# Optimization experiments

Measured on AMD Instinct MI355X. Metric: run time of the kernel, lower is better.

Reference implementation:

```python
import jax, jax.numpy as jnp
import numpy as np

N_NODES = 50000
N_DIRECTED = 800000  # symmetrized to 1.6M (src,dst) pairs
IN_FEAT = 256
HEADS = 8
OUT = 64


def setup_inputs() -> dict:
    key = jax.random.key(0)
    k1, k2, k3, k4, k5 = jax.random.split(key, 5)
    r = jax.random.randint(k1, (N_DIRECTED,), 0, N_NODES)
    c = jax.random.randint(k2, (N_DIRECTED,), 0, N_NODES)
    # symmetric adjacency (values = 1), as edge list
    src = jnp.concatenate([r, c])
    dst = jnp.concatenate([c, r])
    x = jax.random.normal(k3, (N_NODES, IN_FEAT), dtype=jnp.float32)
    Ws = jax.random.normal(k4, (HEADS, OUT, IN_FEAT), dtype=jnp.float32) * 0.05
    As = jax.random.normal(k5, (HEADS, 2 * OUT, 1), dtype=jnp.float32) * 0.05
    return {"x": x, "src": src, "dst": dst, "Ws": Ws, "As": As}


def reference(x, src, dst, Ws, As):
    H, O, F = Ws.shape
    N = x.shape[0]
    # t_nodes = inputs @ Ws^T  -> [H, N, O]
    t = jnp.einsum('nf,hof->hno', x, Ws)
    a_l = As[:, :O, 0]   # [H, O]
    a_r = As[:, O:, 0]   # [H, O]
    Al = jnp.einsum('hno,ho->hn', t, a_l)  # [H, N]
    Ar = jnp.einsum('hno,ho->hn', t, a_r)  # [H, N]
    outs = []
    for k in range(H):
        # sparse E[i,j] = Al[i] + Ar[j] on adjacency pattern
        e = Al[k][src] + Ar[k][dst]  # [E]
        # NOTE: original applies tf.sparse.softmax to E directly (its lrelu
        # tensor is computed but never used), so no leaky_relu here.
        m = jax.ops.segment_max(e, src, num_segments=N)
        ex = jnp.exp(e - m[src])
        den = jax.ops.segment_sum(ex, src, num_segments=N)
        alpha = ex / den[src]
        # sparse_dense_matmul(alphas, t_nodes[k])
        h = jax.ops.segment_sum(alpha[:, None] * t[k][dst], src, num_segments=N)
        outs.append(h)
    out = jnp.stack(outs, axis=1)          # [N, H, O]
    out = out.reshape(N, H * O)            # reduction=False -> concat heads
    return jax.nn.elu(out)
```

## Files before the change

### kernel.cpp

```cpp
#include <hip/hip_runtime.h>
#include <hip/hip_bf16.h>

#define NN 50000
#define INF 256
#define NH 8
#define OUTF 64
#define NC 512
#define NTILES 782
#define EPB 8192
#define NBK 391

typedef __attribute__((ext_vector_type(8))) short bf16x8;
typedef __attribute__((ext_vector_type(4))) float f32x4;
typedef unsigned long long u64;

__device__ __forceinline__ unsigned short f2bf(float f){
  unsigned u = __float_as_uint(f);
  u += 0x7FFFu + ((u>>16)&1u);
  return (unsigned short)(u>>16);
}

#define GLOAD_LDS16(g, s) \
  __builtin_amdgcn_global_load_lds((const __attribute__((address_space(1))) void*)(g), \
                                   (__attribute__((address_space(3))) void*)(s), 16, 0, 0)

__global__ __launch_bounds__(256) void k_prep_w(const float* __restrict__ W,
                                                unsigned short* __restrict__ Wt){
  const int tid = threadIdx.x;
  const int r = tid>>2, cb = (tid&3)*64;
  char* tile = (char*)(Wt + (size_t)blockIdx.x*16384);
  const float* Wr = W + ((long)blockIdx.x*64 + r)*INF;
#pragma unroll
  for (int i=0;i<16;i++){
    int c = cb + i*4;
    float4 v = *(const float4*)(Wr + c);
    ushort4 b; b.x=f2bf(v.x); b.y=f2bf(v.y); b.z=f2bf(v.z); b.w=f2bf(v.w);
    int addr = r*512 + ((((c>>3) ^ (r&7)))<<4) + ((c&7)<<1);
    *(ushort4*)(tile + addr) = b;
  }
}

__global__ void k_atil(const float* __restrict__ W, const float* __restrict__ As,
                       float* __restrict__ atil){
  const int h = blockIdx.x, f = threadIdx.x;
  float s = 0.f;
  for (int o=0;o<64;o++) s += W[((long)h*64+o)*INF + f] * As[h*128 + 64 + o];
  atil[h*256 + f] = s;
}

__global__ __launch_bounds__(256) void k_xbar(const float* __restrict__ x,
                                              const float* __restrict__ atil,
                                              unsigned short* __restrict__ xb,
                                              float* __restrict__ eAr){
  const int tid = threadIdx.x, w = tid>>6, l = tid&63;
  const long n = (long)blockIdx.x*4 + w;
  if (n > NN) return;
  if (n == NN){
    uint2 z; z.x=0; z.y=0;
    *(uint2*)((char*)xb + (size_t)n*512 + l*8) = z;
    if (l < 8) eAr[n*NH + l] = 0.f;
    return;
  }
  float4 v = *(const float4*)(x + n*INF + l*4);
  uint2 d;
  d.x = (unsigned)f2bf(v.x) | ((unsigned)f2bf(v.y)<<16);
  d.y = (unsigned)f2bf(v.z) | ((unsigned)f2bf(v.w)<<16);
  *(uint2*)((char*)xb + (size_t)n*512 + l*8) = d;
  float p[8];
#pragma unroll
  for (int h=0;h<8;h++){
    float4 a = *(const float4*)(atil + h*256 + l*4);
    p[h] = v.x*a.x + v.y*a.y + v.z*a.z + v.w*a.w;
  }
#pragma unroll
  for (int off=1; off<64; off<<=1){
#pragma unroll
    for (int h=0;h<8;h++) p[h] += __shfl_xor(p[h], off, 64);
  }
  if (l < 8){
    float e = p[0];
#pragma unroll
    for (int h=1;h<8;h++) if (l==h) e = p[h];
    eAr[n*NH + l] = __expf(e);
  }
}

__global__ __launch_bounds__(256) void k_bhist(const int* __restrict__ src,
                                               int* __restrict__ M, int E, int NB){
  __shared__ int h[NBK];
  const int tid = threadIdx.x, b = blockIdx.x;
  for (int i=tid;i<NBK;i+=256) h[i]=0;
  __syncthreads();
  const int base = b*EPB;
  const int lim = min(E-base, EPB);
  for (int i=tid;i<lim;i+=256) atomicAdd(&h[src[base+i]>>7], 1);
  __syncthreads();
  for (int i=tid;i<NBK;i+=256) M[(long)i*NB + b] = h[i];
}

__global__ __launch_bounds__(256) void k_bscan(int* __restrict__ M,
                                               int* __restrict__ tot, int NB){
  __shared__ int lds[256];
  const int k = blockIdx.x, tid = threadIdx.x;
  int v = (tid<NB) ? M[(long)k*NB+tid] : 0;
  const int orig = v;
  lds[tid]=v; __syncthreads();
  for (int off=1; off<256; off<<=1){
    int a = (tid>=off)? lds[tid-off] : 0;
    __syncthreads(); lds[tid]+=a; __syncthreads();
  }
  if (tid<NB) M[(long)k*NB+tid] = lds[tid]-orig;
  if (tid==255) tot[k] = lds[255];
}

__global__ __launch_bounds__(512) void k_sscan(const int* __restrict__ in,
                                               int* __restrict__ out, int n){
  __shared__ int lds[512];
  const int tid = threadIdx.x;
  int v = (tid<n)? in[tid] : 0;
  const int orig = v;
  lds[tid]=v; __syncthreads();
  for (int off=1; off<512; off<<=1){
    int a = (tid>=off)? lds[tid-off] : 0;
    __syncthreads(); lds[tid]+=a; __syncthreads();
  }
  if (tid<=n) out[tid] = lds[tid]-orig;
}

__global__ __launch_bounds__(256) void k_bscat(const int* __restrict__ src,
                                               const int* __restrict__ dst,
                                               const int* __restrict__ M,
                                               const int* __restrict__ bOff,
                                               u64* __restrict__ ebuf,
                                               int E, int NB){
  __shared__ int cur[NBK];
  const int tid = threadIdx.x, b = blockIdx.x;
  for (int i=tid;i<NBK;i+=256) cur[i] = bOff[i] + M[(long)i*NB + b];
  __syncthreads();
  const int base = b*EPB;
  const int lim = min(E-base, EPB);
  for (int i=tid;i<lim;i+=256){
    int s = src[base+i], d = dst[base+i];
    int p = atomicAdd(&cur[s>>7], 1);
    ebuf[p] = ((u64)(unsigned)d<<32) | (unsigned)s;
  }
}

__global__ __launch_bounds__(256) void k_bcnt2(const u64* __restrict__ ebuf,
                                               const int* __restrict__ bOff,
                                               int* __restrict__ cnt,
                                               int* __restrict__ pbTot){
  __shared__ int h[128];
  __shared__ int ps[128];
  const int k = blockIdx.x, tid = threadIdx.x;
  if (tid<128) h[tid]=0;
  __syncthreads();
  const int beg = bOff[k], end = bOff[k+1];
  for (int i=beg+tid; i<end; i+=256)
    atomicAdd(&h[(int)(unsigned)ebuf[i] & 127], 1);
  __syncthreads();
  if (tid<128){
    cnt[(k<<7)+tid] = h[tid];
    ps[tid] = (h[tid]+7)&~7;
  }
  __syncthreads();
  for (int off=64; off>0; off>>=1){
    if (tid<off) ps[tid] += ps[tid+off];
    __syncthreads();
  }
  if (tid==0) pbTot[k] = ps[0];
}

__global__ __launch_bounds__(256) void k_final(const u64* __restrict__ ebuf,
                                               const int* __restrict__ bOff,
                                               const int* __restrict__ cnt,
                                               const int* __restrict__ pbOff,
                                               int* __restrict__ row_ptr,
                                               int* __restrict__ col){
  __shared__ int s[128];
  __shared__ int cur[128];
  __shared__ int pend[128];
  const int k = blockIdx.x, tid = threadIdx.x;
  int c = 0, pc = 0;
  if (tid<128){
    c = cnt[(k<<7)+tid];
    pc = (c+7)&~7;
    s[tid] = pc;
  }
  __syncthreads();
  for (int off=1; off<128; off<<=1){
    int a = (tid>=off && tid<128)? s[tid-off] : 0;
    __syncthreads();
    if (tid<128) s[tid] += a;
    __syncthreads();
  }
  const int base = pbOff[k];
  if (tid<128){
    int rp = base + s[tid] - pc;
    row_ptr[(k<<7)+tid] = rp;
    cur[tid] = rp;
    pend[tid] = rp + pc;
  }
  __syncthreads();
  const int beg = bOff[k], end = bOff[k+1];
  for (int i=beg+tid; i<end; i+=256){
    u64 e = ebuf[i];
    int sn = (int)(unsigned)e;
    int d  = (int)(e>>32);
    int p = atomicAdd(&cur[sn&127], 1);
    col[p] = d;
  }
  __syncthreads();
  if (tid<128){
    for (int i=cur[tid]; i<pend[tid]; i++) col[i] = NN;
  }
}

__global__ __launch_bounds__(256) void k_aggr2(const int* __restrict__ row_ptr,
                                               const int* __restrict__ col,
                                               const unsigned short* __restrict__ xb,
                                               const float* __restrict__ eAr,
                                               unsigned short* __restrict__ g,
                                               float* __restrict__ den,
                                               int tile0){
  const int tid = threadIdx.x, l = tid&63;
  const long n = (long)tile0*64 + blockIdx.x*4 + (tid>>6);
  if (n >= NN) return;
  const int beg = __builtin_amdgcn_readfirstlane(row_ptr[n]);
  const int end = __builtin_amdgcn_readfirstlane(row_ptr[n+1]);
  const char* xbp = (const char*)xb;
  float acc[8][4] = {};
  float dnl = 0.f;
  const long l8 = (long)l*8;
  const int lw = l&7;
  for (int i=beg; i<end; i+=8){
    int cc[8];
#pragma unroll
    for (int e=0;e<8;e++) cc[e] = __builtin_amdgcn_readfirstlane(col[i+e]);
    uint2 q[8];
#pragma unroll
    for (int e=0;e<8;e++) q[e] = *(const uint2*)(xbp + (size_t)cc[e]*512 + l8);
    float wl[8];
#pragma unroll
    for (int e=0;e<8;e++) wl[e] = eAr[(size_t)cc[e]*NH + lw];
#pragma unroll
    for (int e=0;e<8;e++) dnl += wl[e];
#pragma unroll
    for (int e=0;e<8;e++){
      const float* we = eAr + (size_t)cc[e]*NH;
      float f0 = __uint_as_float(q[e].x<<16);
      float f1 = __uint_as_float(q[e].x&0xffff0000u);
      float f2 = __uint_as_float(q[e].y<<16);
      float f3 = __uint_as_float(q[e].y&0xffff0000u);
#pragma unroll
      for (int h=0;h<8;h++){
        const float w = we[h];
        acc[h][0] += w*f0; acc[h][1] += w*f1;
        acc[h][2] += w*f2; acc[h][3] += w*f3;
      }
    }
  }
  const int lt = (int)(n>>6) - tile0;
  const int r  = (int)(n&63);
  char* tb = (char*)g + (size_t)lt*262144 + r*512
           + ((((l>>1) ^ (r&7)))<<4) + ((l&1)<<3);
#pragma unroll
  for (int h=0;h<8;h++){
    uint2 d;
    d.x = (unsigned)f2bf(acc[h][0]) | ((unsigned)f2bf(acc[h][1])<<16);
    d.y = (unsigned)f2bf(acc[h][2]) | ((unsigned)f2bf(acc[h][3])<<16);
    *(uint2*)(tb + h*32768) = d;
  }
  if (l < 8) den[n*NH + l] = dnl;
}

__global__ __launch_bounds__(256) void k_gemm2(const unsigned short* __restrict__ g,
                                               const unsigned short* __restrict__ Wt,
                                               const float* __restrict__ den,
                                               float* __restrict__ out,
                                               int tile0){
  __shared__ unsigned short As[16384];
  __shared__ unsigned short Bs[16384];
  __shared__ float linv[64];
  const int tid = threadIdx.x, w = tid>>6, l = tid&63;
  const int brow = tile0 + blockIdx.x;
  const int h = blockIdx.y;
  {
    const char* srcA = (const char*)g + (size_t)blockIdx.x*262144 + h*32768 + w*8192 + l*16;
    char* dstA = (char*)As + w*8192;
#pragma unroll
    for (int k=0;k<8;k++) GLOAD_LDS16(srcA + k*1024, dstA + k*1024);
    const char* srcB = (const char*)Wt + (size_t)h*32768 + w*8192 + l*16;
    char* dstB = (char*)Bs + w*8192;
#pragma unroll
    for (int k=0;k<8;k++) GLOAD_LDS16(srcB + k*1024, dstB + k*1024);
  }
  if (tid < 64){
    long gr = (long)brow*64 + tid;
    float dv = (gr < NN) ? den[gr*NH + h] : 1.f;
    linv[tid] = dv > 0.f ? 1.f/dv : 0.f;
  }
  asm volatile("s_waitcnt vmcnt(0)");
  __syncthreads();

  const int col = w*16 + (l&15);
  f32x4 acc[4] = {};
#pragma unroll
  for (int ks=0; ks<8; ks++){
    int chunkB = (ks*4 + (l>>4)) ^ (col&7);
    bf16x8 bfrag = *(const bf16x8*)((char*)Bs + col*512 + (chunkB<<4));
#pragma unroll
    for (int mt=0; mt<4; mt++){
      int ar_ = mt*16 + (l&15);
      int chunkA = (ks*4 + (l>>4)) ^ (ar_&7);
      bf16x8 afrag = *(const bf16x8*)((char*)As + ar_*512 + (chunkA<<4));
      acc[mt] = __builtin_amdgcn_mfma_f32_16x16x32_bf16(afrag, bfrag, acc[mt], 0,0,0);
    }
  }
#pragma unroll
  for (int mt=0; mt<4; mt++){
#pragma unroll
    for (int j=0;j<4;j++){
      int r = mt*16 + (l>>4)*4 + j;
      long gr = (long)brow*64 + r;
      if (gr < NN){
        float v = acc[mt][j] * linv[r];
        out[gr*NC + h*64 + col] = v>0.f ? v : expm1f(v);
      }
    }
  }
}

extern "C" void kernel_launch(void* const* d_in, const int* in_sizes, int n_in,
                              void* d_out, int out_size, void* d_ws, size_t ws_size,
                              hipStream_t stream){
  const float* x   = (const float*)d_in[0];
  const int*   src = (const int*)d_in[1];
  const int*   dst = (const int*)d_in[2];
  const float* Ws  = (const float*)d_in[3];
  const float* Av  = (const float*)d_in[4];
  const int E = in_sizes[1];
  const int NB = (E + EPB - 1) / EPB;

  char* ws = (char*)d_ws;
  size_t off = 0;
  auto alloc = [&](size_t bytes)->void*{
    void* p = ws + off; off += (bytes + 255) & ~(size_t)255; return p;
  };
  unsigned short* xb   = (unsigned short*)alloc((size_t)50048*512);
  float* eAr           = (float*)alloc((size_t)50048*NH*4);
  float* atil          = (float*)alloc(8*256*4);
  float* den           = (float*)alloc((size_t)50048*NH*4);
  unsigned short* Wt   = (unsigned short*)alloc((size_t)8*32768);
  int*   cnt           = (int*)alloc(50304*4);
  int*   row_ptr       = (int*)alloc(50304*4);
  int*   M             = (int*)alloc((size_t)NBK*256*4);
  int*   tot           = (int*)alloc(512*4);
  int*   bOff          = (int*)alloc(512*4);
  int*   pbTot         = (int*)alloc(512*4);
  int*   pbOff         = (int*)alloc(512*4);
  int*   col           = (int*)alloc(((size_t)E + 8*50048 + 64)*4);

  size_t remain = (ws_size > off + 256) ? (ws_size - off - 256) : 0;
  int chunk = (int)(remain / 262144);
  if (chunk > NTILES) chunk = NTILES;
  if (chunk < 49) chunk = 49;
  unsigned short* g = (unsigned short*)alloc((size_t)chunk*262144);
  u64* ebuf = (u64*)g;

  k_prep_w<<<8,256,0,stream>>>(Ws, Wt);
  k_atil<<<8,256,0,stream>>>(Ws, Av, atil);
  k_xbar<<<12501,256,0,stream>>>(x, atil, xb, eAr);

  k_bhist<<<NB,256,0,stream>>>(src, M, E, NB);
  k_bscan<<<NBK,256,0,stream>>>(M, tot, NB);
  k_sscan<<<1,512,0,stream>>>(tot, bOff, NBK);
  k_bscat<<<NB,256,0,stream>>>(src, dst, M, bOff, ebuf, E, NB);
  k_bcnt2<<<NBK,256,0,stream>>>(ebuf, bOff, cnt, pbTot);
  k_sscan<<<1,512,0,stream>>>(pbTot, pbOff, NBK);
  k_final<<<NBK,256,0,stream>>>(ebuf, bOff, cnt, pbOff, row_ptr, col);

  int tile0 = 0;
  while (tile0 < NTILES){
    int tiles = NTILES - tile0 < chunk ? NTILES - tile0 : chunk;
    k_aggr2<<<tiles*16,256,0,stream>>>(row_ptr, col, xb, eAr, g, den, tile0);
    k_gemm2<<<dim3(tiles,8),256,0,stream>>>(g, Wt, den, (float*)d_out, tile0);
    tile0 += tiles;
  }
}
```

Measured before the change: 337.1 us.

## Split each node's aggregation across two wavefronts and use packed FMA

The aggregation kernel now gives each destination node two wavefronts, each handling half of the 256-wide bf16 feature row. Each lane accumulates 2 features instead of 4 and uses packed v2 FMA, with the per-edge 8-head weights loaded as one vector. The grid doubles to keep coverage. This raises parallelism and cuts per-thread registers to hide gather latency, at the cost of duplicating the col/eAr loads and the denominator work in both wavefronts.

```diff
diff --git a/kernel.cpp b/kernel.cpp
--- a/kernel.cpp
+++ b/kernel.cpp
@@ -12,6 +12,8 @@
 
 typedef __attribute__((ext_vector_type(8))) short bf16x8;
 typedef __attribute__((ext_vector_type(4))) float f32x4;
+typedef __attribute__((ext_vector_type(2))) float v2f;
+typedef __attribute__((ext_vector_type(8))) float f32x8;
 typedef unsigned long long u64;
 
 __device__ __forceinline__ unsigned short f2bf(float f){
@@ -224,22 +226,25 @@
                                                float* __restrict__ den,
                                                int tile0){
   const int tid = threadIdx.x, l = tid&63;
-  const long n = (long)tile0*64 + blockIdx.x*4 + (tid>>6);
+  const int wv = tid>>6;
+  const int fh = wv&1;
+  const long n = (long)tile0*64 + blockIdx.x*2 + (wv>>1);
   if (n >= NN) return;
   const int beg = __builtin_amdgcn_readfirstlane(row_ptr[n]);
   const int end = __builtin_amdgcn_readfirstlane(row_ptr[n+1]);
-  const char* xbp = (const char*)xb;
-  float acc[8][4] = {};
+  const char* xbp = (const char*)xb + fh*256;
+  v2f acc[8] = {};
   float dnl = 0.f;
-  const long l8 = (long)l*8;
+  const long l4 = (long)l*4;
   const int lw = l&7;
+
   for (int i=beg; i<end; i+=8){
     int cc[8];
 #pragma unroll
     for (int e=0;e<8;e++) cc[e] = __builtin_amdgcn_readfirstlane(col[i+e]);
-    uint2 q[8];
-#pragma unroll
-    for (int e=0;e<8;e++) q[e] = *(const uint2*)(xbp + (size_t)cc[e]*512 + l8);
+    unsigned q[8];
+#pragma unroll
+    for (int e=0;e<8;e++) q[e] = *(const unsigned*)(xbp + (size_t)cc[e]*512 + l4);
     float wl[8];
 #pragma unroll
     for (int e=0;e<8;e++) wl[e] = eAr[(size_t)cc[e]*NH + lw];
@@ -247,31 +252,29 @@
     for (int e=0;e<8;e++) dnl += wl[e];
 #pragma unroll
     for (int e=0;e<8;e++){
-      const float* we = eAr + (size_t)cc[e]*NH;
-      float f0 = __uint_as_float(q[e].x<<16);
-      float f1 = __uint_as_float(q[e].x&0xffff0000u);
-      float f2 = __uint_as_float(q[e].y<<16);
-      float f3 = __uint_as_float(q[e].y&0xffff0000u);
+      f32x8 wv8 = *(const f32x8*)(eAr + (size_t)cc[e]*NH);
+      v2f f01;
+      f01.x = __uint_as_float(q[e]<<16);
+      f01.y = __uint_as_float(q[e]&0xffff0000u);
 #pragma unroll
       for (int h=0;h<8;h++){
-        const float w = we[h];
-        acc[h][0] += w*f0; acc[h][1] += w*f1;
-        acc[h][2] += w*f2; acc[h][3] += w*f3;
+        v2f w2; w2.x = wv8[h]; w2.y = wv8[h];
+        acc[h] = __builtin_elementwise_fma(w2, f01, acc[h]);
       }
     }
   }
+
   const int lt = (int)(n>>6) - tile0;
   const int r  = (int)(n&63);
+  const int f0 = fh*128 + l*2;
   char* tb = (char*)g + (size_t)lt*262144 + r*512
-           + ((((l>>1) ^ (r&7)))<<4) + ((l&1)<<3);
+           + ((((f0>>3) ^ (r&7)))<<4) + ((f0&7)<<1);
 #pragma unroll
   for (int h=0;h<8;h++){
-    uint2 d;
-    d.x = (unsigned)f2bf(acc[h][0]) | ((unsigned)f2bf(acc[h][1])<<16);
-    d.y = (unsigned)f2bf(acc[h][2]) | ((unsigned)f2bf(acc[h][3])<<16);
-    *(uint2*)(tb + h*32768) = d;
-  }
-  if (l < 8) den[n*NH + l] = dnl;
+    unsigned d = (unsigned)f2bf(acc[h].x) | ((unsigned)f2bf(acc[h].y)<<16);
+    *(unsigned*)(tb + h*32768) = d;
+  }
+  if (fh==0 && l < 8) den[n*NH + l] = dnl;
 }
 
 __global__ __launch_bounds__(256) void k_gemm2(const unsigned short* __restrict__ g,
@@ -383,7 +386,7 @@
   int tile0 = 0;
   while (tile0 < NTILES){
     int tiles = NTILES - tile0 < chunk ? NTILES - tile0 : chunk;
-    k_aggr2<<<tiles*16,256,0,stream>>>(row_ptr, col, xb, eAr, g, den, tile0);
+    k_aggr2<<<tiles*32,256,0,stream>>>(row_ptr, col, xb, eAr, g, den, tile0);
     k_gemm2<<<dim3(tiles,8),256,0,stream>>>(g, Wt, den, (float*)d_out, tile0);
     tile0 += tiles;
   }
```

New measurement: 329.6 us. 1.02x faster.
